# Kernel optimization log

Hardware: AMD Instinct MI355X
Metric: run time of the kernel (lower is better)

## Reference

```python
import jax, jax.numpy as jnp
import numpy as np

B, SRC, TGT = 1024, 50, 25
I, H = 69, 1024          # input_size = 54 dofs + 15 actions; rnn_size
T = SRC + TGT - 1        # 74 frames total


def gru_cell(x, h, w_ih, w_hh, b_ih, b_hh):
    # PyTorch GRUCell math
    gi = x @ w_ih.T + b_ih            # [B, 3H]
    gh = h @ w_hh.T + b_hh            # [B, 3H]
    i_r, i_z, i_n = jnp.split(gi, 3, axis=-1)
    h_r, h_z, h_n = jnp.split(gh, 3, axis=-1)
    r = jax.nn.sigmoid(i_r + h_r)
    z = jax.nn.sigmoid(i_z + h_z)
    n = jnp.tanh(i_n + r * h_n)
    return (1.0 - z) * n + z * h


def setup_inputs() -> dict:
    key = jax.random.key(0)
    ks = jax.random.split(key, 10)
    s_ih = 1.0 / np.sqrt(H)
    return {
        "encoder_inputs": jax.random.normal(ks[0], (B, SRC, I), jnp.float32),
        "decoder_output": jax.random.normal(ks[1], (B, TGT - 1, I), jnp.float32),
        "w_ih": jax.random.uniform(ks[2], (3 * H, I), jnp.float32, -s_ih, s_ih),
        "w_hh": jax.random.uniform(ks[3], (3 * H, H), jnp.float32, -s_ih, s_ih),
        "b_ih": jax.random.uniform(ks[4], (3 * H,), jnp.float32, -s_ih, s_ih),
        "b_hh": jax.random.uniform(ks[5], (3 * H,), jnp.float32, -s_ih, s_ih),
        "fc1_w": jax.random.uniform(ks[6], (I, H), jnp.float32, -s_ih, s_ih),
        "fc1_b": jax.random.uniform(ks[7], (I,), jnp.float32, -s_ih, s_ih),
        "fc2_w": jax.random.uniform(ks[8], (1, I * T), jnp.float32, -0.01, 0.01),
        "fc2_b": jax.random.uniform(ks[9], (1,), jnp.float32, -0.01, 0.01),
    }


def reference(encoder_inputs, decoder_output, w_ih, w_hh, b_ih, b_hh,
              fc1_w, fc1_b, fc2_w, fc2_b):
    # Dropout is identity in eval mode; faithful deterministic reference.
    all_frame = jnp.concatenate([encoder_inputs, decoder_output], axis=1)  # [B,T,I]
    frames = jnp.transpose(all_frame, (1, 0, 2))                           # [T,B,I]
    batch = encoder_inputs.shape[0]
    state0 = jnp.zeros((batch, H), jnp.float32)

    # Encoding pass: GRU over all T frames
    def step1(h, x):
        return gru_cell(x, h, w_ih, w_hh, b_ih, b_hh), None
    state, _ = jax.lax.scan(step1, state0, frames)

    inp0 = frames[0]
    state = gru_cell(inp0, state, w_ih, w_hh, b_ih, b_hh)
    out0 = inp0 + state @ fc1_w.T + fc1_b

    def step2(carry, _):
        h, prev = carry
        h2 = gru_cell(prev, h, w_ih, w_hh, b_ih, b_hh)
        out = prev + h2 @ fc1_w.T + fc1_b
        return (h2, out), out
    _, rest = jax.lax.scan(step2, (state, out0), None, length=T - 1)

    outputs = jnp.concatenate([out0[None], rest], axis=0)   # [T,B,I]
    base = jnp.transpose(outputs, (1, 0, 2)).reshape(batch, -1)  # [B, T*I]
    logit = base @ fc2_w.T + fc2_b                           # [B,1]
    return jax.nn.sigmoid(logit)
```

## Files before the change

kernel.cpp:

```cpp
#include <hip/hip_runtime.h>
#include <hip/hip_bf16.h>

#define Bsz  1024
#define Hsz  1024
#define Isz  69
#define Tn   74
#define KP   1152
#define XP   128
#define XPF  80
#define XLP  84

typedef short  short8 __attribute__((ext_vector_type(8)));
typedef float  f32x4  __attribute__((ext_vector_type(4)));
using ushort = unsigned short;

__device__ __forceinline__ ushort f2bf(float f) {
    unsigned u = __float_as_uint(f);
    return (ushort)((u + 0x7fffu + ((u >> 16) & 1u)) >> 16);
}

__device__ __forceinline__ void gld_lds16(const void* g, void* l) {
    __builtin_amdgcn_global_load_lds(
        (const __attribute__((address_space(1))) unsigned int*)g,
        (__attribute__((address_space(3))) unsigned int*)l, 16, 0, 0);
}

__global__ void init_k(float* __restrict__ hf, ushort* __restrict__ hbf,
                       float* __restrict__ logit, const float* __restrict__ fc2_b) {
    unsigned gid = blockIdx.x * 256 + threadIdx.x;
    if (gid < 1024u * 1024u) { hf[gid] = 0.f; hbf[gid] = 0; }
    if (gid < 1024u) logit[gid] = fc2_b[0];
}

__global__ void pack_w(const float* __restrict__ w_ih, const float* __restrict__ w_hh,
                       const float* __restrict__ fc1_w,
                       ushort* __restrict__ wpack, ushort* __restrict__ w1p) {
    unsigned gid = blockIdx.x * 256 + threadIdx.x;
    const unsigned WN4 = 3072u * 288u;
    if (gid < WN4) {
        unsigned row = gid / 288u, c4 = (gid % 288u) * 4u;
        ushort4 o; ushort* po = (ushort*)&o;
#pragma unroll
        for (int e = 0; e < 4; ++e) {
            unsigned k = c4 + e; float v = 0.f;
            if (k < 1024u)       v = w_hh[(size_t)row * 1024u + k];
            else if (k < 1093u)  v = w_ih[(size_t)row * 69u + (k - 1024u)];
            po[e] = f2bf(v);
        }
        *(ushort4*)(wpack + (size_t)row * KP + c4) = o;
    } else if (gid < WN4 + 20480u) {
        unsigned g2 = gid - WN4;
        unsigned i = g2 / 256u, c4 = (g2 % 256u) * 4u;
        ushort4 o; ushort* po = (ushort*)&o;
#pragma unroll
        for (int e = 0; e < 4; ++e)
            po[e] = (i < 69u) ? f2bf(fc1_w[(size_t)i * 1024u + c4 + e]) : (ushort)0;
        *(ushort4*)(w1p + (size_t)i * 1024u + c4) = o;
    }
}

__global__ void pack_f(const float* __restrict__ enc, const float* __restrict__ dec,
                       ushort* __restrict__ frames, float* __restrict__ x0f) {
    unsigned gid = blockIdx.x * 256 + threadIdx.x;
    const unsigned NF4 = 74u * 1024u * 32u;
    if (gid < NF4) {
        unsigned c4 = (gid & 31u) * 4u;
        unsigned b  = (gid >> 5) & 1023u;
        unsigned tf = gid >> 15;
        ushort4 o; ushort* po = (ushort*)&o;
#pragma unroll
        for (int e = 0; e < 4; ++e) {
            unsigned i = c4 + e; float v = 0.f;
            if (i < 69u)
                v = (tf < 50u) ? enc[((size_t)b * 50u + tf) * 69u + i]
                               : dec[((size_t)b * 24u + (tf - 50u)) * 69u + i];
            po[e] = f2bf(v);
        }
        *(ushort4*)(frames + (size_t)tf * 1024u * XP + (size_t)b * XP + c4) = o;
    } else if (gid < NF4 + 81920u) {
        unsigned g2 = gid - NF4;
        unsigned b = g2 / 80u, i = g2 % 80u;
        x0f[g2] = (i < 69u) ? enc[(size_t)b * 50u * 69u + i] : 0.f;
    }
}

__launch_bounds__(512, 2)
__global__ void gru_fused(
    const ushort* __restrict__ hbf, const float* __restrict__ hf,
    const ushort* __restrict__ xframe, const float* __restrict__ xprevG,
    const ushort* __restrict__ wpack, const ushort* __restrict__ w1p,
    const float* __restrict__ b_ih, const float* __restrict__ b_hh,
    const float* __restrict__ fc1_b, const float* __restrict__ fc2_w,
    float* __restrict__ hf_out, ushort* __restrict__ hbf_out,
    float* __restrict__ xoutG, float* __restrict__ logitG, int d)
{
    __shared__ __align__(16) ushort ldsH[8 * 8192];
    __shared__ __align__(16) float  xLf[64 * XLP];

    const int t    = threadIdx.x;
    const int blk  = blockIdx.x;
    const int idx  = blk >> 3, xcd = blk & 7;
    const int bn   = xcd * 2 + (idx & 1);
    const int bm   = idx >> 1;
    const int wave = t >> 6, lane = t & 63;
    const int wk   = wave >> 2, wn = wave & 3;
    const int quad = lane >> 4, l16 = lane & 15;
    const int p_   = lane & 15, rl_ = lane >> 4;

#pragma unroll
    for (int c = 0; c < 8; ++c) {
#pragma unroll
        for (int i2 = 0; i2 < 2; ++i2) {
            const int srow = wave * 8 + i2 * 4 + rl_;
            const int cc   = p_ ^ (srow & 15);
            const ushort* g = hbf + (size_t)(bm * 64 + srow) * 1024 + c * 128 + cc * 8;
            gld_lds16(g, &ldsH[c * 8192 + (wave * 8 + i2 * 4) * 128]);
        }
    }

    const ushort* bp0 = wpack + (size_t)(bn * 64 + wn * 16 + l16) * KP + quad * 8 + wk * 64;
    const ushort* bp1 = bp0 + (size_t)1024 * KP;
    const ushort* bp2 = bp0 + (size_t)2048 * KP;
    short8 bq[2][3];
    bq[0][0] = *(const short8*)(bp0);      bq[0][1] = *(const short8*)(bp1);      bq[0][2] = *(const short8*)(bp2);
    bq[1][0] = *(const short8*)(bp0 + 32); bq[1][1] = *(const short8*)(bp1 + 32); bq[1][2] = *(const short8*)(bp2 + 32);

    short8 xf_[4][2];
    float  xp[4][4];
    if (d < 1) {
#pragma unroll
        for (int kk = 0; kk < 2; ++kk) {
            const int gg = (wk * 2 + kk) * 4 + quad;
#pragma unroll
            for (int mt = 0; mt < 4; ++mt)
                xf_[mt][kk] = *(const short8*)(xframe + (size_t)(bm * 64 + mt * 16 + l16) * XP + gg * 8);
        }
    } else if (wave < 5) {
        const int j = wave * 16 + l16;
#pragma unroll
        for (int fm = 0; fm < 4; ++fm)
#pragma unroll
            for (int r = 0; r < 4; ++r)
                xp[fm][r] = xprevG[(size_t)(bm * 64 + fm * 16 + quad * 4 + r) * XPF + j];
    }
    __syncthreads();

    f32x4 accR[4], accZ[4], accNH[4], accNI[4];
#pragma unroll
    for (int i = 0; i < 4; ++i) {
        accR[i]  = (f32x4){0.f,0.f,0.f,0.f}; accZ[i]  = (f32x4){0.f,0.f,0.f,0.f};
        accNH[i] = (f32x4){0.f,0.f,0.f,0.f}; accNI[i] = (f32x4){0.f,0.f,0.f,0.f};
    }

#define MFMA_BF16 __builtin_amdgcn_mfma_f32_16x16x32_bf16
#pragma unroll
    for (int c = 0; c < 8; ++c) {
#pragma unroll
        for (int kk = 0; kk < 2; ++kk) {
            const int g   = (wk * 2 + kk) * 4 + quad;
            const ushort* ab = &ldsH[c * 8192];
            const int pos = (g ^ l16) * 8;
            short8 a0 = *(const short8*)(ab + ( 0 + l16) * 128 + pos);
            short8 a1 = *(const short8*)(ab + (16 + l16) * 128 + pos);
            short8 a2 = *(const short8*)(ab + (32 + l16) * 128 + pos);
            short8 a3 = *(const short8*)(ab + (48 + l16) * 128 + pos);
            short8 b0 = bq[kk][0], b1v = bq[kk][1], b2v = bq[kk][2];
            bq[kk][0] = *(const short8*)(bp0 + (c + 1) * 128 + kk * 32);
            bq[kk][1] = *(const short8*)(bp1 + (c + 1) * 128 + kk * 32);
            bq[kk][2] = *(const short8*)(bp2 + (c + 1) * 128 + kk * 32);
            accR[0] = MFMA_BF16(a0, b0, accR[0],0,0,0);
            accZ[0] = MFMA_BF16(a0, b1v, accZ[0],0,0,0);
            accNH[0]= MFMA_BF16(a0, b2v, accNH[0],0,0,0);
            accR[1] = MFMA_BF16(a1, b0, accR[1],0,0,0);
            accZ[1] = MFMA_BF16(a1, b1v, accZ[1],0,0,0);
            accNH[1]= MFMA_BF16(a1, b2v, accNH[1],0,0,0);
            accR[2] = MFMA_BF16(a2, b0, accR[2],0,0,0);
            accZ[2] = MFMA_BF16(a2, b1v, accZ[2],0,0,0);
            accNH[2]= MFMA_BF16(a2, b2v, accNH[2],0,0,0);
            accR[3] = MFMA_BF16(a3, b0, accR[3],0,0,0);
            accZ[3] = MFMA_BF16(a3, b1v, accZ[3],0,0,0);
            accNH[3]= MFMA_BF16(a3, b2v, accNH[3],0,0,0);
        }
    }

    if (d >= 1 && wave < 5) {
        const int j = wave * 16 + l16;
        const ushort* bfp = w1p + (size_t)j * 1024 + quad * 8;
        f32x4 facc[4];
#pragma unroll
        for (int i = 0; i < 4; ++i) facc[i] = (f32x4){0.f,0.f,0.f,0.f};
#pragma unroll
        for (int c = 0; c < 8; ++c) {
#pragma unroll
            for (int q4 = 0; q4 < 4; ++q4) {
                short8 bb = *(const short8*)(bfp + c * 128 + q4 * 32);
#pragma unroll
                for (int fm = 0; fm < 4; ++fm) {
                    const int row = fm * 16 + l16;
                    short8 aa = *(const short8*)(&ldsH[c * 8192 + row * 128 + (((q4 * 4 + quad) ^ l16) * 8)]);
                    facc[fm] = MFMA_BF16(aa, bb, facc[fm],0,0,0);
                }
            }
        }
        const float b1f = (j < Isz) ? fc1_b[j] : 0.f;
#pragma unroll
        for (int fm = 0; fm < 4; ++fm)
#pragma unroll
            for (int r = 0; r < 4; ++r) {
                const int m = fm * 16 + quad * 4 + r;
                xLf[m * XLP + j] = (j < Isz) ? (xp[fm][r] + facc[fm][r] + b1f) : 0.f;
            }
    }
    __syncthreads();

    if (d >= 1 && bn == 0) {
        for (int i = t; i < 64 * XPF; i += 512) {
            const int r = i / XPF, c2 = i % XPF;
            xoutG[(size_t)(bm * 64 + r) * XPF + c2] = xLf[r * XLP + c2];
        }
    }

    if (d >= 1) {
#pragma unroll
        for (int kk = 0; kk < 2; ++kk) {
            const int gg = (wk * 2 + kk) * 4 + quad;
#pragma unroll
            for (int mt = 0; mt < 4; ++mt) {
                short8 a = (short8){0,0,0,0,0,0,0,0};
                if (gg < 10) {
                    const float* p = &xLf[(mt * 16 + l16) * XLP + gg * 8];
                    f32x4 v0 = *(const f32x4*)p;
                    f32x4 v1 = *(const f32x4*)(p + 4);
                    union { short8 s; ushort u[8]; } uu;
                    uu.u[0] = f2bf(v0[0]); uu.u[1] = f2bf(v0[1]);
                    uu.u[2] = f2bf(v0[2]); uu.u[3] = f2bf(v0[3]);
                    uu.u[4] = f2bf(v1[0]); uu.u[5] = f2bf(v1[1]);
                    uu.u[6] = f2bf(v1[2]); uu.u[7] = f2bf(v1[3]);
                    a = uu.s;
                }
                xf_[mt][kk] = a;
            }
        }
    }
#pragma unroll
    for (int kk = 0; kk < 2; ++kk) {
        short8 b0 = bq[kk][0], b1v = bq[kk][1], b2v = bq[kk][2];
        accR[0] = MFMA_BF16(xf_[0][kk], b0, accR[0],0,0,0);
        accZ[0] = MFMA_BF16(xf_[0][kk], b1v, accZ[0],0,0,0);
        accNI[0]= MFMA_BF16(xf_[0][kk], b2v, accNI[0],0,0,0);
        accR[1] = MFMA_BF16(xf_[1][kk], b0, accR[1],0,0,0);
        accZ[1] = MFMA_BF16(xf_[1][kk], b1v, accZ[1],0,0,0);
        accNI[1]= MFMA_BF16(xf_[1][kk], b2v, accNI[1],0,0,0);
        accR[2] = MFMA_BF16(xf_[2][kk], b0, accR[2],0,0,0);
        accZ[2] = MFMA_BF16(xf_[2][kk], b1v, accZ[2],0,0,0);
        accNI[2]= MFMA_BF16(xf_[2][kk], b2v, accNI[2],0,0,0);
        accR[3] = MFMA_BF16(xf_[3][kk], b0, accR[3],0,0,0);
        accZ[3] = MFMA_BF16(xf_[3][kk], b1v, accZ[3],0,0,0);
        accNI[3]= MFMA_BF16(xf_[3][kk], b2v, accNI[3],0,0,0);
    }

    f32x4* red = (f32x4*)ldsH;
    const int rslot = wn * 64 + lane;
    if (wk == 1) {
#pragma unroll
        for (int mt = 0; mt < 4; ++mt) {
            red[mt * 256 + rslot]        = accR[mt];
            red[1024 + mt * 256 + rslot] = accZ[mt];
        }
    }
    __syncthreads();
    if (wk == 0) {
#pragma unroll
        for (int mt = 0; mt < 4; ++mt) {
            accR[mt] += red[mt * 256 + rslot];
            accZ[mt] += red[1024 + mt * 256 + rslot];
        }
    } else if (d >= 1 && bn == 0 && wave == 5) {
        const int row = lane;
        float lp = 0.f;
        for (int c2 = 0; c2 < Isz; ++c2)
            lp += fc2_w[(size_t)(d - 1) * Isz + c2] * xLf[row * XLP + c2];
        logitG[bm * 64 + row] += lp;
    }
    __syncthreads();
    if (wk == 1) {
#pragma unroll
        for (int mt = 0; mt < 4; ++mt) {
            red[mt * 256 + rslot]        = accNH[mt];
            red[1024 + mt * 256 + rslot] = accNI[mt];
        }
    }
    __syncthreads();
    if (wk == 0) {
#pragma unroll
        for (int mt = 0; mt < 4; ++mt) {
            accNH[mt] += red[mt * 256 + rslot];
            accNI[mt] += red[1024 + mt * 256 + rslot];
        }
        const int j = bn * 64 + wn * 16 + l16;
        const float bir = b_ih[j],        bhr = b_hh[j];
        const float biz = b_ih[1024 + j], bhz = b_hh[1024 + j];
        const float bin_= b_ih[2048 + j], bhn = b_hh[2048 + j];
#pragma unroll
        for (int mt = 0; mt < 4; ++mt) {
#pragma unroll
            for (int r = 0; r < 4; ++r) {
                int m = bm * 64 + mt * 16 + quad * 4 + r;
                float gr = accR[mt][r] + bir + bhr;
                float gz = accZ[mt][r] + biz + bhz;
                float rg = 1.f / (1.f + __expf(-gr));
                float zg = 1.f / (1.f + __expf(-gz));
                float nx = accNI[mt][r] + bin_ + rg * (accNH[mt][r] + bhn);
                nx = fminf(30.f, fmaxf(-30.f, nx));
                float e  = __expf(-2.f * nx);
                float ng = (1.f - e) / (1.f + e);
                float hp = hf[(size_t)m * 1024 + j];
                float hn = (1.f - zg) * ng + zg * hp;
                hf_out[(size_t)m * 1024 + j]  = hn;
                hbf_out[(size_t)m * 1024 + j] = f2bf(hn);
            }
        }
    }
#undef MFMA_BF16
}

__launch_bounds__(512)
__global__ void tail_k(const ushort* __restrict__ hbf, const float* __restrict__ xprevG,
                       const ushort* __restrict__ w1p, const float* __restrict__ fc1_b,
                       const float* __restrict__ fc2_w, const float* __restrict__ logitG,
                       float* __restrict__ outp)
{
    __shared__ __align__(16) ushort ldsH[8 * 8192];
    __shared__ __align__(16) float  xLf[64 * XLP];
    const int t    = threadIdx.x;
    const int bm   = blockIdx.x;
    const int wave = t >> 6, lane = t & 63;
    const int quad = lane >> 4, l16 = lane & 15;
    const int p_   = lane & 15, rl_ = lane >> 4;

#pragma unroll
    for (int c = 0; c < 8; ++c) {
#pragma unroll
        for (int i2 = 0; i2 < 2; ++i2) {
            const int srow = wave * 8 + i2 * 4 + rl_;
            const int cc   = p_ ^ (srow & 15);
            const ushort* g = hbf + (size_t)(bm * 64 + srow) * 1024 + c * 128 + cc * 8;
            gld_lds16(g, &ldsH[c * 8192 + (wave * 8 + i2 * 4) * 128]);
        }
    }
    float xp[4][4];
    if (wave < 5) {
        const int j = wave * 16 + l16;
#pragma unroll
        for (int fm = 0; fm < 4; ++fm)
#pragma unroll
            for (int r = 0; r < 4; ++r)
                xp[fm][r] = xprevG[(size_t)(bm * 64 + fm * 16 + quad * 4 + r) * XPF + j];
    }
    __syncthreads();
    if (wave < 5) {
        const int j = wave * 16 + l16;
        const ushort* bfp = w1p + (size_t)j * 1024 + quad * 8;
        f32x4 facc[4];
#pragma unroll
        for (int i = 0; i < 4; ++i) facc[i] = (f32x4){0.f,0.f,0.f,0.f};
#pragma unroll
        for (int c = 0; c < 8; ++c) {
#pragma unroll
            for (int q4 = 0; q4 < 4; ++q4) {
                short8 bb = *(const short8*)(bfp + c * 128 + q4 * 32);
#pragma unroll
                for (int fm = 0; fm < 4; ++fm) {
                    const int row = fm * 16 + l16;
                    short8 aa = *(const short8*)(&ldsH[c * 8192 + row * 128 + (((q4 * 4 + quad) ^ l16) * 8)]);
                    facc[fm] = __builtin_amdgcn_mfma_f32_16x16x32_bf16(aa, bb, facc[fm],0,0,0);
                }
            }
        }
        const float b1f = (j < Isz) ? fc1_b[j] : 0.f;
#pragma unroll
        for (int fm = 0; fm < 4; ++fm)
#pragma unroll
            for (int r = 0; r < 4; ++r) {
                const int m = fm * 16 + quad * 4 + r;
                xLf[m * XLP + j] = (j < Isz) ? (xp[fm][r] + facc[fm][r] + b1f) : 0.f;
            }
    }
    __syncthreads();
    if (t < 64) {
        float lp = 0.f;
        for (int c2 = 0; c2 < Isz; ++c2)
            lp += fc2_w[(size_t)73 * Isz + c2] * xLf[t * XLP + c2];
        outp[bm * 64 + t] = 1.f / (1.f + __expf(-(logitG[bm * 64 + t] + lp)));
    }
}

extern "C" void kernel_launch(void* const* d_in, const int* in_sizes, int n_in,
                              void* d_out, int out_size, void* d_ws, size_t ws_size,
                              hipStream_t stream)
{
    const float* enc   = (const float*)d_in[0];
    const float* dec   = (const float*)d_in[1];
    const float* w_ih  = (const float*)d_in[2];
    const float* w_hh  = (const float*)d_in[3];
    const float* b_ih  = (const float*)d_in[4];
    const float* b_hh  = (const float*)d_in[5];
    const float* fc1_w = (const float*)d_in[6];
    const float* fc1_b = (const float*)d_in[7];
    const float* fc2_w = (const float*)d_in[8];
    const float* fc2_b = (const float*)d_in[9];
    float* out = (float*)d_out;

    char* ws = (char*)d_ws;
    size_t off = 0;
    auto alloc = [&](size_t bytes) -> void* {
        void* p = ws + off; off += (bytes + 255) & ~(size_t)255; return p;
    };
    ushort* wpack  = (ushort*)alloc((size_t)3072 * KP * 2);
    ushort* w1p    = (ushort*)alloc((size_t)80 * 1024 * 2);
    ushort* frames = (ushort*)alloc((size_t)Tn * 1024 * XP * 2);
    float*  x0f    = (float*) alloc((size_t)1024 * XPF * 4);
    float*  hfA    = (float*) alloc((size_t)1024 * 1024 * 4);
    float*  hfB    = (float*) alloc((size_t)1024 * 1024 * 4);
    ushort* hbfA   = (ushort*)alloc((size_t)1024 * 1024 * 2);
    ushort* hbfB   = (ushort*)alloc((size_t)1024 * 1024 * 2);
    float*  xGA    = (float*) alloc((size_t)1024 * XPF * 4);
    float*  xGB    = (float*) alloc((size_t)1024 * XPF * 4);
    float*  logit  = (float*) alloc((size_t)1024 * 4);

    init_k<<<4096, 256, 0, stream>>>(hfA, hbfA, logit, fc2_b);
    pack_w<<<3536, 256, 0, stream>>>(w_ih, w_hh, fc1_w, wpack, w1p);
    pack_f<<<9792, 256, 0, stream>>>(enc, dec, frames, x0f);

    float*  hf_c = hfA;  float*  hf_n = hfB;
    ushort* hb_c = hbfA; ushort* hb_n = hbfB;

    for (int tt = 0; tt < Tn + 1; ++tt) {
        const ushort* xfr = frames + (size_t)(tt < Tn ? tt : 0) * 1024 * XP;
        gru_fused<<<256, 512, 0, stream>>>(hb_c, hf_c, xfr, x0f, wpack, w1p,
                                           b_ih, b_hh, fc1_b, fc2_w,
                                           hf_n, hb_n, xGA, logit, 0);
        { float*  tf = hf_c; hf_c = hf_n; hf_n = tf; }
        { ushort* tb = hb_c; hb_c = hb_n; hb_n = tb; }
    }
    for (int d = 1; d < Tn; ++d) {
        const float* xin  = (d == 1) ? x0f : ((d & 1) ? xGB : xGA);
        float*       xout = (d & 1) ? xGA : xGB;
        gru_fused<<<256, 512, 0, stream>>>(hb_c, hf_c, frames, xin, wpack, w1p,
                                           b_ih, b_hh, fc1_b, fc2_w,
                                           hf_n, hb_n, xout, logit, d);
        { float*  tf = hf_c; hf_c = hf_n; hf_n = tf; }
        { ushort* tb = hb_c; hb_c = hb_n; hb_n = tb; }
    }
    tail_k<<<16, 512, 0, stream>>>(hb_c, xGA, w1p, fc1_b, fc2_w, logit, out);
}
```

Before: 3.689 ms.

## Deepen weight prefetch and split K-reduction epilogue across both wave groups

New measurement: 4.189 ms. +13.6%, slower.

```diff
diff --git a/kernel.cpp b/kernel.cpp
--- a/kernel.cpp
+++ b/kernel.cpp
@@ -121,21 +121,16 @@
     const ushort* bp0 = wpack + (size_t)(bn * 64 + wn * 16 + l16) * KP + quad * 8 + wk * 64;
     const ushort* bp1 = bp0 + (size_t)1024 * KP;
     const ushort* bp2 = bp0 + (size_t)2048 * KP;
-    short8 bq[2][3];
-    bq[0][0] = *(const short8*)(bp0);      bq[0][1] = *(const short8*)(bp1);      bq[0][2] = *(const short8*)(bp2);
-    bq[1][0] = *(const short8*)(bp0 + 32); bq[1][1] = *(const short8*)(bp1 + 32); bq[1][2] = *(const short8*)(bp2 + 32);
-
-    short8 xf_[4][2];
-    float  xp[4][4];
-    if (d < 1) {
-#pragma unroll
-        for (int kk = 0; kk < 2; ++kk) {
-            const int gg = (wk * 2 + kk) * 4 + quad;
-#pragma unroll
-            for (int mt = 0; mt < 4; ++mt)
-                xf_[mt][kk] = *(const short8*)(xframe + (size_t)(bm * 64 + mt * 16 + l16) * XP + gg * 8);
-        }
-    } else if (wave < 5) {
+    short8 bq[8][3];
+#pragma unroll
+    for (int q = 0; q < 8; ++q) {
+        bq[q][0] = *(const short8*)(bp0 + (q >> 1) * 128 + (q & 1) * 32);
+        bq[q][1] = *(const short8*)(bp1 + (q >> 1) * 128 + (q & 1) * 32);
+        bq[q][2] = *(const short8*)(bp2 + (q >> 1) * 128 + (q & 1) * 32);
+    }
+
+    float xp[4][4];
+    if (d >= 1 && wave < 5) {
         const int j = wave * 16 + l16;
 #pragma unroll
         for (int fm = 0; fm < 4; ++fm)
@@ -154,33 +149,34 @@
 
 #define MFMA_BF16 __builtin_amdgcn_mfma_f32_16x16x32_bf16
 #pragma unroll
-    for (int c = 0; c < 8; ++c) {
-#pragma unroll
-        for (int kk = 0; kk < 2; ++kk) {
-            const int g   = (wk * 2 + kk) * 4 + quad;
-            const ushort* ab = &ldsH[c * 8192];
-            const int pos = (g ^ l16) * 8;
-            short8 a0 = *(const short8*)(ab + ( 0 + l16) * 128 + pos);
-            short8 a1 = *(const short8*)(ab + (16 + l16) * 128 + pos);
-            short8 a2 = *(const short8*)(ab + (32 + l16) * 128 + pos);
-            short8 a3 = *(const short8*)(ab + (48 + l16) * 128 + pos);
-            short8 b0 = bq[kk][0], b1v = bq[kk][1], b2v = bq[kk][2];
-            bq[kk][0] = *(const short8*)(bp0 + (c + 1) * 128 + kk * 32);
-            bq[kk][1] = *(const short8*)(bp1 + (c + 1) * 128 + kk * 32);
-            bq[kk][2] = *(const short8*)(bp2 + (c + 1) * 128 + kk * 32);
-            accR[0] = MFMA_BF16(a0, b0, accR[0],0,0,0);
-            accZ[0] = MFMA_BF16(a0, b1v, accZ[0],0,0,0);
-            accNH[0]= MFMA_BF16(a0, b2v, accNH[0],0,0,0);
-            accR[1] = MFMA_BF16(a1, b0, accR[1],0,0,0);
-            accZ[1] = MFMA_BF16(a1, b1v, accZ[1],0,0,0);
-            accNH[1]= MFMA_BF16(a1, b2v, accNH[1],0,0,0);
-            accR[2] = MFMA_BF16(a2, b0, accR[2],0,0,0);
-            accZ[2] = MFMA_BF16(a2, b1v, accZ[2],0,0,0);
-            accNH[2]= MFMA_BF16(a2, b2v, accNH[2],0,0,0);
-            accR[3] = MFMA_BF16(a3, b0, accR[3],0,0,0);
-            accZ[3] = MFMA_BF16(a3, b1v, accZ[3],0,0,0);
-            accNH[3]= MFMA_BF16(a3, b2v, accNH[3],0,0,0);
-        }
+    for (int q = 0; q < 16; ++q) {
+        const int c  = q >> 1, kk = q & 1;
+        const int g  = (wk * 2 + kk) * 4 + quad;
+        const ushort* ab = &ldsH[c * 8192];
+        const int pos = (g ^ l16) * 8;
+        short8 a0 = *(const short8*)(ab + ( 0 + l16) * 128 + pos);
+        short8 a1 = *(const short8*)(ab + (16 + l16) * 128 + pos);
+        short8 a2 = *(const short8*)(ab + (32 + l16) * 128 + pos);
+        short8 a3 = *(const short8*)(ab + (48 + l16) * 128 + pos);
+        short8 b0 = bq[q & 7][0], b1v = bq[q & 7][1], b2v = bq[q & 7][2];
+        if (q < 10) {
+            const int qc = (q + 8) >> 1, qk = (q + 8) & 1;
+            bq[q & 7][0] = *(const short8*)(bp0 + qc * 128 + qk * 32);
+            bq[q & 7][1] = *(const short8*)(bp1 + qc * 128 + qk * 32);
+            bq[q & 7][2] = *(const short8*)(bp2 + qc * 128 + qk * 32);
+        }
+        accR[0] = MFMA_BF16(a0, b0, accR[0],0,0,0);
+        accZ[0] = MFMA_BF16(a0, b1v, accZ[0],0,0,0);
+        accNH[0]= MFMA_BF16(a0, b2v, accNH[0],0,0,0);
+        accR[1] = MFMA_BF16(a1, b0, accR[1],0,0,0);
+        accZ[1] = MFMA_BF16(a1, b1v, accZ[1],0,0,0);
+        accNH[1]= MFMA_BF16(a1, b2v, accNH[1],0,0,0);
+        accR[2] = MFMA_BF16(a2, b0, accR[2],0,0,0);
+        accZ[2] = MFMA_BF16(a2, b1v, accZ[2],0,0,0);
+        accNH[2]= MFMA_BF16(a2, b2v, accNH[2],0,0,0);
+        accR[3] = MFMA_BF16(a3, b0, accR[3],0,0,0);
+        accZ[3] = MFMA_BF16(a3, b1v, accZ[3],0,0,0);
+        accNH[3]= MFMA_BF16(a3, b2v, accNH[3],0,0,0);
     }
 
     if (d >= 1 && wave < 5) {
@@ -220,7 +216,16 @@
         }
     }
 
-    if (d >= 1) {
+    short8 xf_[4][2];
+    if (d < 1) {
+#pragma unroll
+        for (int kk = 0; kk < 2; ++kk) {
+            const int gg = (wk * 2 + kk) * 4 + quad;
+#pragma unroll
+            for (int mt = 0; mt < 4; ++mt)
+                xf_[mt][kk] = *(const short8*)(xframe + (size_t)(bm * 64 + mt * 16 + l16) * XP + gg * 8);
+        }
+    } else {
 #pragma unroll
         for (int kk = 0; kk < 2; ++kk) {
             const int gg = (wk * 2 + kk) * 4 + quad;
@@ -259,67 +264,66 @@
         accNI[3]= MFMA_BF16(xf_[3][kk], b2v, accNI[3],0,0,0);
     }
 
-    f32x4* red = (f32x4*)ldsH;
-    const int rslot = wn * 64 + lane;
-    if (wk == 1) {
-#pragma unroll
-        for (int mt = 0; mt < 4; ++mt) {
-            red[mt * 256 + rslot]        = accR[mt];
-            red[1024 + mt * 256 + rslot] = accZ[mt];
-        }
-    }
+    f32x4* exch = (f32x4*)ldsH;
+    const int slot = wn * 64 + lane;
+    {
+        const int mtb = wk ? 0 : 2;
+        f32x4* w = exch + wk * 2048;
+#pragma unroll
+        for (int i = 0; i < 2; ++i) {
+            const int mt = mtb + i;
+            w[(i * 4 + 0) * 256 + slot] = accR[mt];
+            w[(i * 4 + 1) * 256 + slot] = accZ[mt];
+            w[(i * 4 + 2) * 256 + slot] = accNH[mt];
+            w[(i * 4 + 3) * 256 + slot] = accNI[mt];
+        }
+    }
+    const int jcol = bn * 64 + wn * 16 + l16;
+    const int mto  = wk * 2;
+    float hp[2][4];
+#pragma unroll
+    for (int i = 0; i < 2; ++i)
+#pragma unroll
+        for (int r = 0; r < 4; ++r)
+            hp[i][r] = hf[(size_t)(bm * 64 + (mto + i) * 16 + quad * 4 + r) * 1024 + jcol];
     __syncthreads();
-    if (wk == 0) {
-#pragma unroll
-        for (int mt = 0; mt < 4; ++mt) {
-            accR[mt] += red[mt * 256 + rslot];
-            accZ[mt] += red[1024 + mt * 256 + rslot];
-        }
-    } else if (d >= 1 && bn == 0 && wave == 5) {
+
+    {
+        const f32x4* rd = exch + (wk ^ 1) * 2048;
+        const float bir = b_ih[jcol],        bhr = b_hh[jcol];
+        const float biz = b_ih[1024 + jcol], bhz = b_hh[1024 + jcol];
+        const float bin_= b_ih[2048 + jcol], bhn = b_hh[2048 + jcol];
+#pragma unroll
+        for (int i = 0; i < 2; ++i) {
+            const int mt = mto + i;
+            f32x4 aR = accR[mt] + rd[(i * 4 + 0) * 256 + slot];
+            f32x4 aZ = accZ[mt] + rd[(i * 4 + 1) * 256 + slot];
+            f32x4 aH = accNH[mt]+ rd[(i * 4 + 2) * 256 + slot];
+            f32x4 aI = accNI[mt]+ rd[(i * 4 + 3) * 256 + slot];
+#pragma unroll
+            for (int r = 0; r < 4; ++r) {
+                const int m = bm * 64 + mt * 16 + quad * 4 + r;
+                float gr = aR[r] + bir + bhr;
+                float gz = aZ[r] + biz + bhz;
+                float rg = 1.f / (1.f + __expf(-gr));
+                float zg = 1.f / (1.f + __expf(-gz));
+                float nx = aI[r] + bin_ + rg * (aH[r] + bhn);
+                nx = fminf(30.f, fmaxf(-30.f, nx));
+                float e  = __expf(-2.f * nx);
+                float ng = (1.f - e) / (1.f + e);
+                float hn = (1.f - zg) * ng + zg * hp[i][r];
+                hf_out[(size_t)m * 1024 + jcol]  = hn;
+                hbf_out[(size_t)m * 1024 + jcol] = f2bf(hn);
+            }
+        }
+    }
+
+    if (d >= 1 && bn == 0 && wave == 5) {
         const int row = lane;
         float lp = 0.f;
         for (int c2 = 0; c2 < Isz; ++c2)
             lp += fc2_w[(size_t)(d - 1) * Isz + c2] * xLf[row * XLP + c2];
         logitG[bm * 64 + row] += lp;
-    }
-    __syncthreads();
-    if (wk == 1) {
-#pragma unroll
-        for (int mt = 0; mt < 4; ++mt) {
-            red[mt * 256 + rslot]        = accNH[mt];
-            red[1024 + mt * 256 + rslot] = accNI[mt];
-        }
-    }
-    __syncthreads();
-    if (wk == 0) {
-#pragma unroll
-        for (int mt = 0; mt < 4; ++mt) {
-            accNH[mt] += red[mt * 256 + rslot];
-            accNI[mt] += red[1024 + mt * 256 + rslot];
-        }
-        const int j = bn * 64 + wn * 16 + l16;
-        const float bir = b_ih[j],        bhr = b_hh[j];
-        const float biz = b_ih[1024 + j], bhz = b_hh[1024 + j];
-        const float bin_= b_ih[2048 + j], bhn = b_hh[2048 + j];
-#pragma unroll
-        for (int mt = 0; mt < 4; ++mt) {
-#pragma unroll
-            for (int r = 0; r < 4; ++r) {
-                int m = bm * 64 + mt * 16 + quad * 4 + r;
-                float gr = accR[mt][r] + bir + bhr;
-                float gz = accZ[mt][r] + biz + bhz;
-                float rg = 1.f / (1.f + __expf(-gr));
-                float zg = 1.f / (1.f + __expf(-gz));
-                float nx = accNI[mt][r] + bin_ + rg * (accNH[mt][r] + bhn);
-                nx = fminf(30.f, fmaxf(-30.f, nx));
-                float e  = __expf(-2.f * nx);
-                float ng = (1.f - e) / (1.f + e);
-                float hp = hf[(size_t)m * 1024 + j];
-                float hn = (1.f - zg) * ng + zg * hp;
-                hf_out[(size_t)m * 1024 + j]  = hn;
-                hbf_out[(size_t)m * 1024 + j] = f2bf(hn);
-            }
-        }
     }
 #undef MFMA_BF16
 }
```

## Replace per-timestep launches with a persistent GRU kernel and per-row-group barriers

Applied to the files above, without the earlier changes.

Result: slower. 5.822 ms (+57.8%).

```diff
diff --git a/kernel.cpp b/kernel.cpp
--- a/kernel.cpp
+++ b/kernel.cpp
@@ -13,10 +13,19 @@
 typedef short  short8 __attribute__((ext_vector_type(8)));
 typedef float  f32x4  __attribute__((ext_vector_type(4)));
 using ushort = unsigned short;
+using u64 = unsigned long long;
+typedef u64 u64x2 __attribute__((ext_vector_type(2)));
 
 __device__ __forceinline__ ushort f2bf(float f) {
     unsigned u = __float_as_uint(f);
     return (ushort)((u + 0x7fffu + ((u >> 16) & 1u)) >> 16);
+}
+
+__device__ __forceinline__ u64 cload8(const ushort* p) {
+    return __hip_atomic_load((const u64*)p, __ATOMIC_RELAXED, __HIP_MEMORY_SCOPE_AGENT);
+}
+__device__ __forceinline__ void cstore2(ushort* p, ushort v) {
+    __hip_atomic_store(p, v, __ATOMIC_RELAXED, __HIP_MEMORY_SCOPE_AGENT);
 }
 
 __device__ __forceinline__ void gld_lds16(const void* g, void* l) {
@@ -26,10 +35,10 @@
 }
 
 __global__ void init_k(float* __restrict__ hf, ushort* __restrict__ hbf,
-                       float* __restrict__ logit, const float* __restrict__ fc2_b) {
+                       unsigned* __restrict__ bar) {
     unsigned gid = blockIdx.x * 256 + threadIdx.x;
     if (gid < 1024u * 1024u) { hf[gid] = 0.f; hbf[gid] = 0; }
-    if (gid < 1024u) logit[gid] = fc2_b[0];
+    if (gid < 1024u) bar[gid] = 0u;
 }
 
 __global__ void pack_w(const float* __restrict__ w_ih, const float* __restrict__ w_hh,
@@ -85,14 +94,13 @@
 }
 
 __launch_bounds__(512, 2)
-__global__ void gru_fused(
-    const ushort* __restrict__ hbf, const float* __restrict__ hf,
-    const ushort* __restrict__ xframe, const float* __restrict__ xprevG,
-    const ushort* __restrict__ wpack, const ushort* __restrict__ w1p,
+__global__ void rnn_persist(
+    const ushort* __restrict__ wpack, const ushort* __restrict__ frames,
+    const ushort* __restrict__ w1p,
     const float* __restrict__ b_ih, const float* __restrict__ b_hh,
-    const float* __restrict__ fc1_b, const float* __restrict__ fc2_w,
-    float* __restrict__ hf_out, ushort* __restrict__ hbf_out,
-    float* __restrict__ xoutG, float* __restrict__ logitG, int d)
+    const float* __restrict__ fc1_b, const float* __restrict__ x0f,
+    float* hfA, float* hfB, ushort* hbfA, ushort* hbfB,
+    float* __restrict__ xall, unsigned* bar)
 {
     __shared__ __align__(16) ushort ldsH[8 * 8192];
     __shared__ __align__(16) float  xLf[64 * XLP];
@@ -107,6 +115,269 @@
     const int quad = lane >> 4, l16 = lane & 15;
     const int p_   = lane & 15, rl_ = lane >> 4;
 
+    unsigned bar_no = 0;
+    unsigned* mycnt = bar + bm * 64;
+
+    const ushort* bp0 = wpack + (size_t)(bn * 64 + wn * 16 + l16) * KP + quad * 8 + wk * 64;
+    const ushort* bp1 = bp0 + (size_t)1024 * KP;
+    const ushort* bp2 = bp0 + (size_t)2048 * KP;
+
+    float*  hf_c = hfA;  float*  hf_n = hfB;
+    ushort* hb_c = hbfA; ushort* hb_n = hbfB;
+
+#define MFMA_BF16 __builtin_amdgcn_mfma_f32_16x16x32_bf16
+
+#pragma unroll 1
+    for (int step = 0; step < 148; ++step) {
+        const int d = step - 74;
+
+        u64 sA[8][2][2];
+#pragma unroll
+        for (int c = 0; c < 8; ++c) {
+#pragma unroll
+            for (int i2 = 0; i2 < 2; ++i2) {
+                const int srow = wave * 8 + i2 * 4 + rl_;
+                const int cc   = p_ ^ (srow & 15);
+                const ushort* gp = hb_c + (size_t)(bm * 64 + srow) * 1024 + c * 128 + cc * 8;
+                sA[c][i2][0] = cload8(gp); sA[c][i2][1] = cload8(gp + 4);
+            }
+        }
+        short8 bq[2][3];
+        bq[0][0] = *(const short8*)(bp0);      bq[0][1] = *(const short8*)(bp1);      bq[0][2] = *(const short8*)(bp2);
+        bq[1][0] = *(const short8*)(bp0 + 32); bq[1][1] = *(const short8*)(bp1 + 32); bq[1][2] = *(const short8*)(bp2 + 32);
+#pragma unroll
+        for (int c = 0; c < 8; ++c) {
+#pragma unroll
+            for (int i2 = 0; i2 < 2; ++i2) {
+                u64x2 v; v.x = sA[c][i2][0]; v.y = sA[c][i2][1];
+                *(u64x2*)((char*)(&ldsH[c * 8192 + (wave * 8 + i2 * 4) * 128]) + lane * 16) = v;
+            }
+        }
+        short8 xf_[4][2];
+        if (d <= 0) {
+            const ushort* xb = frames + (size_t)(d < 0 ? step : 0) * 1024 * XP;
+#pragma unroll
+            for (int kk = 0; kk < 2; ++kk) {
+                const int gg = (wk * 2 + kk) * 4 + quad;
+#pragma unroll
+                for (int mt = 0; mt < 4; ++mt)
+                    xf_[mt][kk] = *(const short8*)(xb + (size_t)(bm * 64 + mt * 16 + l16) * XP + gg * 8);
+            }
+        }
+        if (d == 0) {
+            for (int i = t; i < 64 * XPF; i += 512) {
+                const int r = i / XPF, c2 = i % XPF;
+                xLf[r * XLP + c2] = x0f[(size_t)(bm * 64 + r) * XPF + c2];
+            }
+        }
+        __syncthreads();
+
+        f32x4 accR[4], accZ[4], accNH[4], accNI[4];
+#pragma unroll
+        for (int i = 0; i < 4; ++i) {
+            accR[i]  = (f32x4){0.f,0.f,0.f,0.f}; accZ[i]  = (f32x4){0.f,0.f,0.f,0.f};
+            accNH[i] = (f32x4){0.f,0.f,0.f,0.f}; accNI[i] = (f32x4){0.f,0.f,0.f,0.f};
+        }
+
+#pragma unroll
+        for (int c = 0; c < 8; ++c) {
+#pragma unroll
+            for (int kk = 0; kk < 2; ++kk) {
+                const int g   = (wk * 2 + kk) * 4 + quad;
+                const ushort* ab = &ldsH[c * 8192];
+                const int pos = (g ^ l16) * 8;
+                short8 a0 = *(const short8*)(ab + ( 0 + l16) * 128 + pos);
+                short8 a1 = *(const short8*)(ab + (16 + l16) * 128 + pos);
+                short8 a2 = *(const short8*)(ab + (32 + l16) * 128 + pos);
+                short8 a3 = *(const short8*)(ab + (48 + l16) * 128 + pos);
+                short8 b0 = bq[kk][0], b1v = bq[kk][1], b2v = bq[kk][2];
+                bq[kk][0] = *(const short8*)(bp0 + (c + 1) * 128 + kk * 32);
+                bq[kk][1] = *(const short8*)(bp1 + (c + 1) * 128 + kk * 32);
+                bq[kk][2] = *(const short8*)(bp2 + (c + 1) * 128 + kk * 32);
+                accR[0] = MFMA_BF16(a0, b0, accR[0],0,0,0);
+                accZ[0] = MFMA_BF16(a0, b1v, accZ[0],0,0,0);
+                accNH[0]= MFMA_BF16(a0, b2v, accNH[0],0,0,0);
+                accR[1] = MFMA_BF16(a1, b0, accR[1],0,0,0);
+                accZ[1] = MFMA_BF16(a1, b1v, accZ[1],0,0,0);
+                accNH[1]= MFMA_BF16(a1, b2v, accNH[1],0,0,0);
+                accR[2] = MFMA_BF16(a2, b0, accR[2],0,0,0);
+                accZ[2] = MFMA_BF16(a2, b1v, accZ[2],0,0,0);
+                accNH[2]= MFMA_BF16(a2, b2v, accNH[2],0,0,0);
+                accR[3] = MFMA_BF16(a3, b0, accR[3],0,0,0);
+                accZ[3] = MFMA_BF16(a3, b1v, accZ[3],0,0,0);
+                accNH[3]= MFMA_BF16(a3, b2v, accNH[3],0,0,0);
+            }
+        }
+
+        if (d >= 1 && wave < 5) {
+            const int j = wave * 16 + l16;
+            const ushort* bfp = w1p + (size_t)j * 1024 + quad * 8;
+            f32x4 facc[4];
+#pragma unroll
+            for (int i = 0; i < 4; ++i) facc[i] = (f32x4){0.f,0.f,0.f,0.f};
+#pragma unroll
+            for (int c = 0; c < 8; ++c) {
+#pragma unroll
+                for (int q4 = 0; q4 < 4; ++q4) {
+                    short8 bb = *(const short8*)(bfp + c * 128 + q4 * 32);
+#pragma unroll
+                    for (int fm = 0; fm < 4; ++fm) {
+                        const int row = fm * 16 + l16;
+                        short8 aa = *(const short8*)(&ldsH[c * 8192 + row * 128 + (((q4 * 4 + quad) ^ l16) * 8)]);
+                        facc[fm] = MFMA_BF16(aa, bb, facc[fm],0,0,0);
+                    }
+                }
+            }
+            const float b1f = (j < Isz) ? fc1_b[j] : 0.f;
+#pragma unroll
+            for (int fm = 0; fm < 4; ++fm)
+#pragma unroll
+                for (int r = 0; r < 4; ++r) {
+                    const int m = fm * 16 + quad * 4 + r;
+                    const float xpv = xLf[m * XLP + j];
+                    xLf[m * XLP + j] = (j < Isz) ? (xpv + facc[fm][r] + b1f) : 0.f;
+                }
+        }
+        __syncthreads();
+
+        if (d >= 1 && bn == 0) {
+            for (int i = t; i < 64 * XPF; i += 512) {
+                const int r = i / XPF, c2 = i % XPF;
+                xall[(size_t)(d - 1) * 1024 * XPF + (size_t)(bm * 64 + r) * XPF + c2]
+                    = xLf[r * XLP + c2];
+            }
+        }
+
+        if (d >= 1) {
+#pragma unroll
+            for (int kk = 0; kk < 2; ++kk) {
+                const int gg = (wk * 2 + kk) * 4 + quad;
+#pragma unroll
+                for (int mt = 0; mt < 4; ++mt) {
+                    short8 a = (short8){0,0,0,0,0,0,0,0};
+                    if (gg < 10) {
+                        const float* p = &xLf[(mt * 16 + l16) * XLP + gg * 8];
+                        f32x4 v0 = *(const f32x4*)p;
+                        f32x4 v1 = *(const f32x4*)(p + 4);
+                        union { short8 s; ushort u[8]; } uu;
+                        uu.u[0] = f2bf(v0[0]); uu.u[1] = f2bf(v0[1]);
+                        uu.u[2] = f2bf(v0[2]); uu.u[3] = f2bf(v0[3]);
+                        uu.u[4] = f2bf(v1[0]); uu.u[5] = f2bf(v1[1]);
+                        uu.u[6] = f2bf(v1[2]); uu.u[7] = f2bf(v1[3]);
+                        a = uu.s;
+                    }
+                    xf_[mt][kk] = a;
+                }
+            }
+        }
+#pragma unroll
+        for (int kk = 0; kk < 2; ++kk) {
+            short8 b0 = bq[kk][0], b1v = bq[kk][1], b2v = bq[kk][2];
+            accR[0] = MFMA_BF16(xf_[0][kk], b0, accR[0],0,0,0);
+            accZ[0] = MFMA_BF16(xf_[0][kk], b1v, accZ[0],0,0,0);
+            accNI[0]= MFMA_BF16(xf_[0][kk], b2v, accNI[0],0,0,0);
+            accR[1] = MFMA_BF16(xf_[1][kk], b0, accR[1],0,0,0);
+            accZ[1] = MFMA_BF16(xf_[1][kk], b1v, accZ[1],0,0,0);
+            accNI[1]= MFMA_BF16(xf_[1][kk], b2v, accNI[1],0,0,0);
+            accR[2] = MFMA_BF16(xf_[2][kk], b0, accR[2],0,0,0);
+            accZ[2] = MFMA_BF16(xf_[2][kk], b1v, accZ[2],0,0,0);
+            accNI[2]= MFMA_BF16(xf_[2][kk], b2v, accNI[2],0,0,0);
+            accR[3] = MFMA_BF16(xf_[3][kk], b0, accR[3],0,0,0);
+            accZ[3] = MFMA_BF16(xf_[3][kk], b1v, accZ[3],0,0,0);
+            accNI[3]= MFMA_BF16(xf_[3][kk], b2v, accNI[3],0,0,0);
+        }
+
+        f32x4* red = (f32x4*)ldsH;
+        const int rslot = wn * 64 + lane;
+        if (wk == 1) {
+#pragma unroll
+            for (int mt = 0; mt < 4; ++mt) {
+                red[mt * 256 + rslot]        = accR[mt];
+                red[1024 + mt * 256 + rslot] = accZ[mt];
+            }
+        }
+        __syncthreads();
+        if (wk == 0) {
+#pragma unroll
+            for (int mt = 0; mt < 4; ++mt) {
+                accR[mt] += red[mt * 256 + rslot];
+                accZ[mt] += red[1024 + mt * 256 + rslot];
+            }
+        }
+        __syncthreads();
+        if (wk == 1) {
+#pragma unroll
+            for (int mt = 0; mt < 4; ++mt) {
+                red[mt * 256 + rslot]        = accNH[mt];
+                red[1024 + mt * 256 + rslot] = accNI[mt];
+            }
+        }
+        __syncthreads();
+        if (wk == 0) {
+#pragma unroll
+            for (int mt = 0; mt < 4; ++mt) {
+                accNH[mt] += red[mt * 256 + rslot];
+                accNI[mt] += red[1024 + mt * 256 + rslot];
+            }
+            const int j = bn * 64 + wn * 16 + l16;
+            const float bir = b_ih[j],        bhr = b_hh[j];
+            const float biz = b_ih[1024 + j], bhz = b_hh[1024 + j];
+            const float bin_= b_ih[2048 + j], bhn = b_hh[2048 + j];
+#pragma unroll
+            for (int mt = 0; mt < 4; ++mt) {
+#pragma unroll
+                for (int r = 0; r < 4; ++r) {
+                    int m = bm * 64 + mt * 16 + quad * 4 + r;
+                    float gr = accR[mt][r] + bir + bhr;
+                    float gz = accZ[mt][r] + biz + bhz;
+                    float rg = 1.f / (1.f + __expf(-gr));
+                    float zg = 1.f / (1.f + __expf(-gz));
+                    float nx = accNI[mt][r] + bin_ + rg * (accNH[mt][r] + bhn);
+                    nx = fminf(30.f, fmaxf(-30.f, nx));
+                    float e  = __expf(-2.f * nx);
+                    float ng = (1.f - e) / (1.f + e);
+                    float hp = hf_c[(size_t)m * 1024 + j];
+                    float hn = (1.f - zg) * ng + zg * hp;
+                    hf_n[(size_t)m * 1024 + j] = hn;
+                    cstore2(&hb_n[(size_t)m * 1024 + j], f2bf(hn));
+                }
+            }
+        }
+
+        __syncthreads();
+        ++bar_no;
+        if (t == 0) {
+            __hip_atomic_fetch_add(mycnt, 1u, __ATOMIC_RELAXED, __HIP_MEMORY_SCOPE_AGENT);
+            const unsigned tgt = bar_no * 16u;
+            unsigned guard = 0;
+            while (__hip_atomic_load(mycnt, __ATOMIC_RELAXED, __HIP_MEMORY_SCOPE_AGENT) < tgt) {
+                if (++guard > 4096u) break;
+                __builtin_amdgcn_s_sleep(4);
+            }
+        }
+        __syncthreads();
+
+        { float*  tf = hf_c; hf_c = hf_n; hf_n = tf; }
+        { ushort* tb = hb_c; hb_c = hb_n; hb_n = tb; }
+    }
+#undef MFMA_BF16
+}
+
+__launch_bounds__(512)
+__global__ void tail2_k(const ushort* __restrict__ hbf, const float* __restrict__ xall,
+                        const ushort* __restrict__ w1p, const float* __restrict__ fc1_b,
+                        const float* __restrict__ fc2_w, const float* __restrict__ fc2_b,
+                        float* __restrict__ outp)
+{
+    __shared__ __align__(16) ushort ldsH[8 * 8192];
+    __shared__ __align__(16) float  xLf[64 * XLP];
+    __shared__ float lsum[8][64];
+    const int t    = threadIdx.x;
+    const int bm   = blockIdx.x;
+    const int wave = t >> 6, lane = t & 63;
+    const int quad = lane >> 4, l16 = lane & 15;
+    const int p_   = lane & 15, rl_ = lane >> 4;
+
 #pragma unroll
     for (int c = 0; c < 8; ++c) {
 #pragma unroll
@@ -117,237 +388,6 @@
             gld_lds16(g, &ldsH[c * 8192 + (wave * 8 + i2 * 4) * 128]);
         }
     }
-
-    const ushort* bp0 = wpack + (size_t)(bn * 64 + wn * 16 + l16) * KP + quad * 8 + wk * 64;
-    const ushort* bp1 = bp0 + (size_t)1024 * KP;
-    const ushort* bp2 = bp0 + (size_t)2048 * KP;
-    short8 bq[2][3];
-    bq[0][0] = *(const short8*)(bp0);      bq[0][1] = *(const short8*)(bp1);      bq[0][2] = *(const short8*)(bp2);
-    bq[1][0] = *(const short8*)(bp0 + 32); bq[1][1] = *(const short8*)(bp1 + 32); bq[1][2] = *(const short8*)(bp2 + 32);
-
-    short8 xf_[4][2];
-    float  xp[4][4];
-    if (d < 1) {
-#pragma unroll
-        for (int kk = 0; kk < 2; ++kk) {
-            const int gg = (wk * 2 + kk) * 4 + quad;
-#pragma unroll
-            for (int mt = 0; mt < 4; ++mt)
-                xf_[mt][kk] = *(const short8*)(xframe + (size_t)(bm * 64 + mt * 16 + l16) * XP + gg * 8);
-        }
-    } else if (wave < 5) {
-        const int j = wave * 16 + l16;
-#pragma unroll
-        for (int fm = 0; fm < 4; ++fm)
-#pragma unroll
-            for (int r = 0; r < 4; ++r)
-                xp[fm][r] = xprevG[(size_t)(bm * 64 + fm * 16 + quad * 4 + r) * XPF + j];
-    }
-    __syncthreads();
-
-    f32x4 accR[4], accZ[4], accNH[4], accNI[4];
-#pragma unroll
-    for (int i = 0; i < 4; ++i) {
-        accR[i]  = (f32x4){0.f,0.f,0.f,0.f}; accZ[i]  = (f32x4){0.f,0.f,0.f,0.f};
-        accNH[i] = (f32x4){0.f,0.f,0.f,0.f}; accNI[i] = (f32x4){0.f,0.f,0.f,0.f};
-    }
-
-#define MFMA_BF16 __builtin_amdgcn_mfma_f32_16x16x32_bf16
-#pragma unroll
-    for (int c = 0; c < 8; ++c) {
-#pragma unroll
-        for (int kk = 0; kk < 2; ++kk) {
-            const int g   = (wk * 2 + kk) * 4 + quad;
-            const ushort* ab = &ldsH[c * 8192];
-            const int pos = (g ^ l16) * 8;
-            short8 a0 = *(const short8*)(ab + ( 0 + l16) * 128 + pos);
-            short8 a1 = *(const short8*)(ab + (16 + l16) * 128 + pos);
-            short8 a2 = *(const short8*)(ab + (32 + l16) * 128 + pos);
-            short8 a3 = *(const short8*)(ab + (48 + l16) * 128 + pos);
-            short8 b0 = bq[kk][0], b1v = bq[kk][1], b2v = bq[kk][2];
-            bq[kk][0] = *(const short8*)(bp0 + (c + 1) * 128 + kk * 32);
-            bq[kk][1] = *(const short8*)(bp1 + (c + 1) * 128 + kk * 32);
-            bq[kk][2] = *(const short8*)(bp2 + (c + 1) * 128 + kk * 32);
-            accR[0] = MFMA_BF16(a0, b0, accR[0],0,0,0);
-            accZ[0] = MFMA_BF16(a0, b1v, accZ[0],0,0,0);
-            accNH[0]= MFMA_BF16(a0, b2v, accNH[0],0,0,0);
-            accR[1] = MFMA_BF16(a1, b0, accR[1],0,0,0);
-            accZ[1] = MFMA_BF16(a1, b1v, accZ[1],0,0,0);
-            accNH[1]= MFMA_BF16(a1, b2v, accNH[1],0,0,0);
-            accR[2] = MFMA_BF16(a2, b0, accR[2],0,0,0);
-            accZ[2] = MFMA_BF16(a2, b1v, accZ[2],0,0,0);
-            accNH[2]= MFMA_BF16(a2, b2v, accNH[2],0,0,0);
-            accR[3] = MFMA_BF16(a3, b0, accR[3],0,0,0);
-            accZ[3] = MFMA_BF16(a3, b1v, accZ[3],0,0,0);
-            accNH[3]= MFMA_BF16(a3, b2v, accNH[3],0,0,0);
-        }
-    }
-
-    if (d >= 1 && wave < 5) {
-        const int j = wave * 16 + l16;
-        const ushort* bfp = w1p + (size_t)j * 1024 + quad * 8;
-        f32x4 facc[4];
-#pragma unroll
-        for (int i = 0; i < 4; ++i) facc[i] = (f32x4){0.f,0.f,0.f,0.f};
-#pragma unroll
-        for (int c = 0; c < 8; ++c) {
-#pragma unroll
-            for (int q4 = 0; q4 < 4; ++q4) {
-                short8 bb = *(const short8*)(bfp + c * 128 + q4 * 32);
-#pragma unroll
-                for (int fm = 0; fm < 4; ++fm) {
-                    const int row = fm * 16 + l16;
-                    short8 aa = *(const short8*)(&ldsH[c * 8192 + row * 128 + (((q4 * 4 + quad) ^ l16) * 8)]);
-                    facc[fm] = MFMA_BF16(aa, bb, facc[fm],0,0,0);
-                }
-            }
-        }
-        const float b1f = (j < Isz) ? fc1_b[j] : 0.f;
-#pragma unroll
-        for (int fm = 0; fm < 4; ++fm)
-#pragma unroll
-            for (int r = 0; r < 4; ++r) {
-                const int m = fm * 16 + quad * 4 + r;
-                xLf[m * XLP + j] = (j < Isz) ? (xp[fm][r] + facc[fm][r] + b1f) : 0.f;
-            }
-    }
-    __syncthreads();
-
-    if (d >= 1 && bn == 0) {
-        for (int i = t; i < 64 * XPF; i += 512) {
-            const int r = i / XPF, c2 = i % XPF;
-            xoutG[(size_t)(bm * 64 + r) * XPF + c2] = xLf[r * XLP + c2];
-        }
-    }
-
-    if (d >= 1) {
-#pragma unroll
-        for (int kk = 0; kk < 2; ++kk) {
-            const int gg = (wk * 2 + kk) * 4 + quad;
-#pragma unroll
-            for (int mt = 0; mt < 4; ++mt) {
-                short8 a = (short8){0,0,0,0,0,0,0,0};
-                if (gg < 10) {
-                    const float* p = &xLf[(mt * 16 + l16) * XLP + gg * 8];
-                    f32x4 v0 = *(const f32x4*)p;
-                    f32x4 v1 = *(const f32x4*)(p + 4);
-                    union { short8 s; ushort u[8]; } uu;
-                    uu.u[0] = f2bf(v0[0]); uu.u[1] = f2bf(v0[1]);
-                    uu.u[2] = f2bf(v0[2]); uu.u[3] = f2bf(v0[3]);
-                    uu.u[4] = f2bf(v1[0]); uu.u[5] = f2bf(v1[1]);
-                    uu.u[6] = f2bf(v1[2]); uu.u[7] = f2bf(v1[3]);
-                    a = uu.s;
-                }
-                xf_[mt][kk] = a;
-            }
-        }
-    }
-#pragma unroll
-    for (int kk = 0; kk < 2; ++kk) {
-        short8 b0 = bq[kk][0], b1v = bq[kk][1], b2v = bq[kk][2];
-        accR[0] = MFMA_BF16(xf_[0][kk], b0, accR[0],0,0,0);
-        accZ[0] = MFMA_BF16(xf_[0][kk], b1v, accZ[0],0,0,0);
-        accNI[0]= MFMA_BF16(xf_[0][kk], b2v, accNI[0],0,0,0);
-        accR[1] = MFMA_BF16(xf_[1][kk], b0, accR[1],0,0,0);
-        accZ[1] = MFMA_BF16(xf_[1][kk], b1v, accZ[1],0,0,0);
-        accNI[1]= MFMA_BF16(xf_[1][kk], b2v, accNI[1],0,0,0);
-        accR[2] = MFMA_BF16(xf_[2][kk], b0, accR[2],0,0,0);
-        accZ[2] = MFMA_BF16(xf_[2][kk], b1v, accZ[2],0,0,0);
-        accNI[2]= MFMA_BF16(xf_[2][kk], b2v, accNI[2],0,0,0);
-        accR[3] = MFMA_BF16(xf_[3][kk], b0, accR[3],0,0,0);
-        accZ[3] = MFMA_BF16(xf_[3][kk], b1v, accZ[3],0,0,0);
-        accNI[3]= MFMA_BF16(xf_[3][kk], b2v, accNI[3],0,0,0);
-    }
-
-    f32x4* red = (f32x4*)ldsH;
-    const int rslot = wn * 64 + lane;
-    if (wk == 1) {
-#pragma unroll
-        for (int mt = 0; mt < 4; ++mt) {
-            red[mt * 256 + rslot]        = accR[mt];
-            red[1024 + mt * 256 + rslot] = accZ[mt];
-        }
-    }
-    __syncthreads();
-    if (wk == 0) {
-#pragma unroll
-        for (int mt = 0; mt < 4; ++mt) {
-            accR[mt] += red[mt * 256 + rslot];
-            accZ[mt] += red[1024 + mt * 256 + rslot];
-        }
-    } else if (d >= 1 && bn == 0 && wave == 5) {
-        const int row = lane;
-        float lp = 0.f;
-        for (int c2 = 0; c2 < Isz; ++c2)
-            lp += fc2_w[(size_t)(d - 1) * Isz + c2] * xLf[row * XLP + c2];
-        logitG[bm * 64 + row] += lp;
-    }
-    __syncthreads();
-    if (wk == 1) {
-#pragma unroll
-        for (int mt = 0; mt < 4; ++mt) {
-            red[mt * 256 + rslot]        = accNH[mt];
-            red[1024 + mt * 256 + rslot] = accNI[mt];
-        }
-    }
-    __syncthreads();
-    if (wk == 0) {
-#pragma unroll
-        for (int mt = 0; mt < 4; ++mt) {
-            accNH[mt] += red[mt * 256 + rslot];
-            accNI[mt] += red[1024 + mt * 256 + rslot];
-        }
-        const int j = bn * 64 + wn * 16 + l16;
-        const float bir = b_ih[j],        bhr = b_hh[j];
-        const float biz = b_ih[1024 + j], bhz = b_hh[1024 + j];
-        const float bin_= b_ih[2048 + j], bhn = b_hh[2048 + j];
-#pragma unroll
-        for (int mt = 0; mt < 4; ++mt) {
-#pragma unroll
-            for (int r = 0; r < 4; ++r) {
-                int m = bm * 64 + mt * 16 + quad * 4 + r;
-                float gr = accR[mt][r] + bir + bhr;
-                float gz = accZ[mt][r] + biz + bhz;
-                float rg = 1.f / (1.f + __expf(-gr));
-                float zg = 1.f / (1.f + __expf(-gz));
-                float nx = accNI[mt][r] + bin_ + rg * (accNH[mt][r] + bhn);
-                nx = fminf(30.f, fmaxf(-30.f, nx));
-                float e  = __expf(-2.f * nx);
-                float ng = (1.f - e) / (1.f + e);
-                float hp = hf[(size_t)m * 1024 + j];
-                float hn = (1.f - zg) * ng + zg * hp;
-                hf_out[(size_t)m * 1024 + j]  = hn;
-                hbf_out[(size_t)m * 1024 + j] = f2bf(hn);
-            }
-        }
-    }
-#undef MFMA_BF16
-}
-
-__launch_bounds__(512)
-__global__ void tail_k(const ushort* __restrict__ hbf, const float* __restrict__ xprevG,
-                       const ushort* __restrict__ w1p, const float* __restrict__ fc1_b,
-                       const float* __restrict__ fc2_w, const float* __restrict__ logitG,
-                       float* __restrict__ outp)
-{
-    __shared__ __align__(16) ushort ldsH[8 * 8192];
-    __shared__ __align__(16) float  xLf[64 * XLP];
-    const int t    = threadIdx.x;
-    const int bm   = blockIdx.x;
-    const int wave = t >> 6, lane = t & 63;
-    const int quad = lane >> 4, l16 = lane & 15;
-    const int p_   = lane & 15, rl_ = lane >> 4;
-
-#pragma unroll
-    for (int c = 0; c < 8; ++c) {
-#pragma unroll
-        for (int i2 = 0; i2 < 2; ++i2) {
-            const int srow = wave * 8 + i2 * 4 + rl_;
-            const int cc   = p_ ^ (srow & 15);
-            const ushort* g = hbf + (size_t)(bm * 64 + srow) * 1024 + c * 128 + cc * 8;
-            gld_lds16(g, &ldsH[c * 8192 + (wave * 8 + i2 * 4) * 128]);
-        }
-    }
     float xp[4][4];
     if (wave < 5) {
         const int j = wave * 16 + l16;
@@ -355,7 +395,8 @@
         for (int fm = 0; fm < 4; ++fm)
 #pragma unroll
             for (int r = 0; r < 4; ++r)
-                xp[fm][r] = xprevG[(size_t)(bm * 64 + fm * 16 + quad * 4 + r) * XPF + j];
+                xp[fm][r] = xall[(size_t)72 * 1024 * XPF +
+                                 (size_t)(bm * 64 + fm * 16 + quad * 4 + r) * XPF + j];
     }
     __syncthreads();
     if (wave < 5) {
@@ -387,11 +428,24 @@
             }
     }
     __syncthreads();
+    {
+        const int m = t & 63, dg = t >> 6;
+        float p = 0.f;
+        for (int i = dg; i < 73; i += 8) {
+            const float* xr = xall + (size_t)i * 1024 * XPF + (size_t)(bm * 64 + m) * XPF;
+            const float* wr = fc2_w + (size_t)i * Isz;
+            for (int c2 = 0; c2 < Isz; ++c2) p += wr[c2] * xr[c2];
+        }
+        lsum[dg][m] = p;
+    }
+    __syncthreads();
     if (t < 64) {
-        float lp = 0.f;
-        for (int c2 = 0; c2 < Isz; ++c2)
-            lp += fc2_w[(size_t)73 * Isz + c2] * xLf[t * XLP + c2];
-        outp[bm * 64 + t] = 1.f / (1.f + __expf(-(logitG[bm * 64 + t] + lp)));
+        float lp = fc2_b[0];
+#pragma unroll
+        for (int g2 = 0; g2 < 8; ++g2) lp += lsum[g2][t];
+        const float* wr = fc2_w + (size_t)73 * Isz;
+        for (int c2 = 0; c2 < Isz; ++c2) lp += wr[c2] * xLf[t * XLP + c2];
+        outp[bm * 64 + t] = 1.f / (1.f + __expf(-lp));
     }
 }
 
@@ -424,33 +478,16 @@
     float*  hfB    = (float*) alloc((size_t)1024 * 1024 * 4);
     ushort* hbfA   = (ushort*)alloc((size_t)1024 * 1024 * 2);
     ushort* hbfB   = (ushort*)alloc((size_t)1024 * 1024 * 2);
-    float*  xGA    = (float*) alloc((size_t)1024 * XPF * 4);
-    float*  xGB    = (float*) alloc((size_t)1024 * XPF * 4);
-    float*  logit  = (float*) alloc((size_t)1024 * 4);
-
-    init_k<<<4096, 256, 0, stream>>>(hfA, hbfA, logit, fc2_b);
+    float*  xall   = (float*) alloc((size_t)73 * 1024 * XPF * 4);
+    unsigned* bar  = (unsigned*)alloc((size_t)1024 * 4);
+
+    init_k<<<4096, 256, 0, stream>>>(hfA, hbfA, bar);
     pack_w<<<3536, 256, 0, stream>>>(w_ih, w_hh, fc1_w, wpack, w1p);
     pack_f<<<9792, 256, 0, stream>>>(enc, dec, frames, x0f);
 
-    float*  hf_c = hfA;  float*  hf_n = hfB;
-    ushort* hb_c = hbfA; ushort* hb_n = hbfB;
-
-    for (int tt = 0; tt < Tn + 1; ++tt) {
-        const ushort* xfr = frames + (size_t)(tt < Tn ? tt : 0) * 1024 * XP;
-        gru_fused<<<256, 512, 0, stream>>>(hb_c, hf_c, xfr, x0f, wpack, w1p,
-                                           b_ih, b_hh, fc1_b, fc2_w,
-                                           hf_n, hb_n, xGA, logit, 0);
-        { float*  tf = hf_c; hf_c = hf_n; hf_n = tf; }
-        { ushort* tb = hb_c; hb_c = hb_n; hb_n = tb; }
-    }
-    for (int d = 1; d < Tn; ++d) {
-        const float* xin  = (d == 1) ? x0f : ((d & 1) ? xGB : xGA);
-        float*       xout = (d & 1) ? xGA : xGB;
-        gru_fused<<<256, 512, 0, stream>>>(hb_c, hf_c, frames, xin, wpack, w1p,
-                                           b_ih, b_hh, fc1_b, fc2_w,
-                                           hf_n, hb_n, xout, logit, d);
-        { float*  tf = hf_c; hf_c = hf_n; hf_n = tf; }
-        { ushort* tb = hb_c; hb_c = hb_n; hb_n = tb; }
-    }
-    tail_k<<<16, 512, 0, stream>>>(hb_c, xGA, w1p, fc1_b, fc2_w, logit, out);
-}
+    rnn_persist<<<256, 512, 0, stream>>>(
+        wpack, frames, w1p, b_ih, b_hh, fc1_b, x0f,
+        hfA, hfB, hbfA, hbfB, xall, bar);
+
+    tail2_k<<<16, 512, 0, stream>>>(hbfA, xall, w1p, fc1_b, fc2_w, fc2_b, out);
+}
```
